# Performance work log

Hardware: AMD Instinct MI355X
Metric: run time of the kernel (lower is better)

Reference implementation:

```python
import jax, jax.numpy as jnp
import numpy as np

DOWNSAMPLE = 4
OUT_RATIO = 8


def _avg_pool(x, k):
    b, c, h, w = x.shape
    return x.reshape(b, c, h // k, k, w // k, k).mean(axis=(3, 5))


def _upsample_axis(x, axis, scale):
    # bilinear, align_corners=True along one axis
    n = x.shape[axis]
    m = n * scale
    coords = jnp.arange(m, dtype=x.dtype) * ((n - 1) / (m - 1))
    i0 = jnp.floor(coords).astype(jnp.int32)
    i1 = jnp.minimum(i0 + 1, n - 1)
    f = coords - i0.astype(x.dtype)
    x0 = jnp.take(x, i0, axis=axis)
    x1 = jnp.take(x, i1, axis=axis)
    shp = [1] * x.ndim
    shp[axis] = m
    f = f.reshape(shp)
    return x0 * (1 - f) + x1 * f


def _upsample_bilinear(x, scale):
    return _upsample_axis(_upsample_axis(x, 2, scale), 3, scale)


def _conv1x1(x, W, b):
    # x: (b,c,h,w), W: (out,in), b: (out,)
    return jnp.einsum('bchw,oc->bohw', x, W) + b[None, :, None, None]


def setup_inputs() -> dict:
    key = jax.random.key(0)
    ks = jax.random.split(key, 8)
    C = 64
    Cq = C // OUT_RATIO
    s = 1.0 / np.sqrt(C)
    x = jax.random.normal(ks[0], (8, C, 256, 256), dtype=jnp.float32)
    Wq = jax.random.uniform(ks[1], (Cq, C), jnp.float32, -s, s)
    bq = jax.random.uniform(ks[2], (Cq,), jnp.float32, -s, s)
    Wk = jax.random.uniform(ks[3], (Cq, C), jnp.float32, -s, s)
    bk = jax.random.uniform(ks[4], (Cq,), jnp.float32, -s, s)
    Wv = jax.random.uniform(ks[5], (C, C), jnp.float32, -s, s)
    bv = jax.random.uniform(ks[6], (C,), jnp.float32, -s, s)
    gamma = jax.random.normal(ks[7], (1,), jnp.float32) * 0.1
    return {"x": x, "Wq": Wq, "bq": bq, "Wk": Wk, "bk": bk, "Wv": Wv, "bv": bv, "gamma": gamma}


def reference(x, Wq, bq, Wk, bk, Wv, bv, gamma):
    b, c, h, w = x.shape
    xd = _avg_pool(x, DOWNSAMPLE)          # (b, c, hd, wd)
    hd, wd = xd.shape[2], xd.shape[3]
    n = hd * wd
    q = _conv1x1(xd, Wq, bq).reshape(b, -1, n)   # (b, cq, n)
    k = _conv1x1(xd, Wk, bk).reshape(b, -1, n)   # (b, cq, n)
    v = _conv1x1(xd, Wv, bv).reshape(b, c, n)    # (b, c, n)
    energy = jnp.einsum('bci,bcj->bij', q, k)    # (b, n, n), no scaling (as in source)
    attn = jax.nn.softmax(energy, axis=-1)
    out = jnp.einsum('bcj,bij->bci', v, attn)    # out[b,c,i] = sum_j v[b,c,j]*attn[b,i,j]
    out = out.reshape(b, c, hd, wd)
    out = _upsample_bilinear(out, DOWNSAMPLE)    # back to (b, c, h, w)
    return gamma[0] * out + x
```

## Files before the change

kernel.cpp:

```cpp
#include <hip/hip_runtime.h>
#include <hip/hip_bf16.h>

#define CCH 64
#define NPIX 4096
#define LOG2E 1.4426950408889634f

typedef __attribute__((ext_vector_type(8))) short short8;
typedef __attribute__((ext_vector_type(16))) float f32x16;

union U4S8 { uint4 u; short8 s; };

__device__ inline uint32_t pk2bf(float lo, float hi) {
    __hip_bfloat162 h = __float22bfloat162_rn(make_float2(lo, hi));
    return *reinterpret_cast<uint32_t*>(&h);
}

__global__ __launch_bounds__(256, 4) void pool_conv_kernel(
    const float* __restrict__ x,
    const float* __restrict__ Wq, const float* __restrict__ bq,
    const float* __restrict__ Wk, const float* __restrict__ bk,
    const float* __restrict__ Wv, const float* __restrict__ bv,
    __hip_bfloat16* __restrict__ Qo, __hip_bfloat16* __restrict__ Ko,
    __hip_bfloat16* __restrict__ VPo)
{
    const int blk  = blockIdx.x;
    const int b    = blk >> 7;
    const int prow = (blk >> 1) & 63;
    const int half = blk & 1;
    const int t    = threadIdx.x;
    const int lane = t & 63;
    const int w    = t >> 6;
    const int l31  = lane & 31;
    const int hi   = lane >> 5;

    __shared__ __align__(16) __hip_bfloat16 xdt[32][72];
    __shared__ __align__(16) __hip_bfloat16 otile[80][36];
    __shared__ float sbias[96];

    if (t < 96) {
        float v = 0.f;
        if (t < 8)       v = bq[t];
        else if (t < 16) v = bk[t-8];
        else if (t < 80) v = bv[t-16];
        sbias[t] = v;
    }

    const float* xbase = x + (((size_t)(b*CCH))*256 + (size_t)(prow*4 + hi))*256
                           + half*128 + l31*4;
    #pragma unroll
    for (int cc = 0; cc < 16; ++cc) {
        const int c = w*16 + cc;
        const float* xp = xbase + (size_t)c*65536;
        float4 a0 = *(const float4*)(xp);
        float4 a1 = *(const float4*)(xp + 512);
        float s = (a0.x+a0.y+a0.z+a0.w) + (a1.x+a1.y+a1.z+a1.w);
        s += __shfl_xor(s, 32);
        if (hi == 0) xdt[l31][c] = __float2bfloat16(s * 0.0625f);
    }

    const int  oct  = w;
    const bool busy = (w < 3);
    short8 wf[4];
    if (busy) {
        const int row = oct*32 + l31;
        const float* wr = nullptr;
        if (row < 8)       wr = Wq + row*CCH;
        else if (row < 16) wr = Wk + (row-8)*CCH;
        else if (row < 80) wr = Wv + (row-16)*CCH;
        #pragma unroll
        for (int kt = 0; kt < 4; ++kt) {
            U4S8 f;
            if (wr) {
                const int c0 = kt*16 + hi*8;
                float4 a = *(const float4*)(wr + c0);
                float4 d = *(const float4*)(wr + c0 + 4);
                f.u.x = pk2bf(a.x, a.y); f.u.y = pk2bf(a.z, a.w);
                f.u.z = pk2bf(d.x, d.y); f.u.w = pk2bf(d.z, d.w);
            } else {
                f.u = make_uint4(0,0,0,0);
            }
            wf[kt] = f.s;
        }
    }

    __syncthreads();

    if (busy) {
        short8 xf[4];
        #pragma unroll
        for (int kt = 0; kt < 4; ++kt)
            xf[kt] = *(const short8*)&xdt[l31][kt*16 + hi*8];

        f32x16 acc;
        #pragma unroll
        for (int r = 0; r < 16; ++r) acc[r] = 0.f;
        #pragma unroll
        for (int kt = 0; kt < 4; ++kt)
            acc = __builtin_amdgcn_mfma_f32_32x32x16_bf16(wf[kt], xf[kt], acc, 0, 0, 0);

        #pragma unroll
        for (int r = 0; r < 16; ++r) {
            const int row = (r&3) + 8*(r>>2) + 4*hi;
            const int oc  = oct*32 + row;
            if (oc < 80) {
                float v = acc[r] + sbias[oc];
                if (oc < 8) v *= LOG2E;
                otile[oc][l31] = __float2bfloat16(v);
            }
        }
    }
    __syncthreads();

    const int i0 = prow*64 + half*32;
    if (t < 64) {
        const int p = t & 31;
        const int oc0 = (t < 32) ? 0 : 8;
        unsigned short v[8];
        #pragma unroll
        for (int j = 0; j < 8; ++j)
            v[j] = *reinterpret_cast<const unsigned short*>(&otile[oc0 + j][p]);
        uint4 q;
        q.x = (uint32_t)v[0] | ((uint32_t)v[1] << 16);
        q.y = (uint32_t)v[2] | ((uint32_t)v[3] << 16);
        q.z = (uint32_t)v[4] | ((uint32_t)v[5] << 16);
        q.w = (uint32_t)v[6] | ((uint32_t)v[7] << 16);
        __hip_bfloat16* dst = (t < 32) ? Qo : Ko;
        *(uint4*)(dst + ((size_t)b*NPIX + i0 + p)*8) = q;
    }
    {
        const int chg = i0 >> 5;
        __hip_bfloat16* vdst = VPo + ((size_t)b*512 + (size_t)chg*4)*512;
        const int f   = t >> 6;
        const int s1  = f >> 1;
        const int ct  = f & 1;
        const int l   = t & 63;
        const int c31 = l & 31;
        const int h2  = l >> 5;
        const int row = 16 + ct*32 + c31;
        const int pt0 = s1*16 + h2*4;
        uint2 a0 = *(const uint2*)&otile[row][pt0];
        uint2 a1 = *(const uint2*)&otile[row][pt0 + 8];
        *(uint4*)(vdst + t*8) = make_uint4(a0.x, a0.y, a1.x, a1.y);
    }
}

__global__ __launch_bounds__(256, 4) void attn_kernel(
    const __hip_bfloat16* __restrict__ Q, const __hip_bfloat16* __restrict__ K,
    const __hip_bfloat16* __restrict__ VP, float* __restrict__ OS)
{
    const int bb   = blockIdx.x;
    const int b    = bb & 7;
    const int qg   = bb >> 3;
    const int i0   = qg * 32;
    const int t    = threadIdx.x;
    const int lane = t & 63;
    const int kvq  = t >> 6;
    const int l31  = lane & 31;
    const int hi   = lane >> 5;

    __shared__ float tiles[4][64][33];
    __shared__ float ml[4][32];
    __shared__ float ils[32];

    U4S8 qf;
    if (hi == 0) qf.u = *(const uint4*)(Q + ((size_t)b*NPIX + i0 + l31)*8);
    else         qf.u = make_uint4(0,0,0,0);

    f32x16 acc0, acc1, zacc;
    #pragma unroll
    for (int r = 0; r < 16; ++r) { acc0[r] = 0.f; acc1[r] = 0.f; zacc[r] = 0.f; }
    float l = 0.f;

    const __hip_bfloat16* Kb  = K  + (size_t)b*NPIX*8;
    const __hip_bfloat16* VPb = VP + (size_t)b*512*512;

    auto ldK = [&](int kv) {
        U4S8 r;
        if (hi == 0) r.u = *(const uint4*)(Kb + (size_t)(kv + l31)*8);
        else         r.u = make_uint4(0,0,0,0);
        return r;
    };
    auto ldVP = [&](int chg, int s1, int ct) {
        U4S8 r;
        r.u = *(const uint4*)(VPb + ((size_t)((chg*2 + s1)*2 + ct))*512 + lane*8);
        return r;
    };

    int kv0 = kvq * 1024;
    U4S8 kf = ldK(kv0);
    U4S8 v00 = ldVP(kv0>>5, 0, 0), v10 = ldVP(kv0>>5, 0, 1);
    U4S8 v01 = ldVP(kv0>>5, 1, 0), v11 = ldVP(kv0>>5, 1, 1);

    #pragma unroll 1
    for (int ch = 0; ch < 32; ++ch) {
        U4S8 ckf = kf, cv00 = v00, cv01 = v01, cv10 = v10, cv11 = v11;
        const int nkv0 = kv0 + 32;
        kf  = ldK(nkv0);
        v00 = ldVP(nkv0>>5, 0, 0); v10 = ldVP(nkv0>>5, 0, 1);
        v01 = ldVP(nkv0>>5, 1, 0); v11 = ldVP(nkv0>>5, 1, 1);

        f32x16 s = __builtin_amdgcn_mfma_f32_32x32x16_bf16(ckf.s, qf.s, zacc, 0, 0, 0);

        float p[16];
        float ssum = 0.f;
        #pragma unroll
        for (int r = 0; r < 16; ++r) { p[r] = __builtin_exp2f(s[r]); ssum += p[r]; }
        l += ssum;

        U4S8 pb0, pb1;
        pb0.u.x = pk2bf(p[0],  p[1]);  pb0.u.y = pk2bf(p[2],  p[3]);
        pb0.u.z = pk2bf(p[4],  p[5]);  pb0.u.w = pk2bf(p[6],  p[7]);
        pb1.u.x = pk2bf(p[8],  p[9]);  pb1.u.y = pk2bf(p[10], p[11]);
        pb1.u.z = pk2bf(p[12], p[13]); pb1.u.w = pk2bf(p[14], p[15]);

        acc0 = __builtin_amdgcn_mfma_f32_32x32x16_bf16(cv00.s, pb0.s, acc0, 0, 0, 0);
        acc1 = __builtin_amdgcn_mfma_f32_32x32x16_bf16(cv10.s, pb0.s, acc1, 0, 0, 0);
        acc0 = __builtin_amdgcn_mfma_f32_32x32x16_bf16(cv01.s, pb1.s, acc0, 0, 0, 0);
        acc1 = __builtin_amdgcn_mfma_f32_32x32x16_bf16(cv11.s, pb1.s, acc1, 0, 0, 0);

        kv0 = nkv0;
    }

    l += __shfl_xor(l, 32);

    #pragma unroll
    for (int r = 0; r < 16; ++r) {
        const int cr = (r&3) + 8*(r>>2) + 4*hi;
        tiles[kvq][cr]     [l31] = acc0[r];
        tiles[kvq][cr + 32][l31] = acc1[r];
    }
    if (hi == 0) ml[kvq][l31] = l;
    __syncthreads();

    if (t < 32) ils[t] = 1.f / (ml[0][t] + ml[1][t] + ml[2][t] + ml[3][t]);
    __syncthreads();

    float* outp = OS + (size_t)b*CCH*NPIX + i0;
    const int c  = t >> 2;
    const int q8 = (t & 3) * 8;
    float o[8];
    #pragma unroll
    for (int j = 0; j < 8; ++j) {
        const int q = q8 + j;
        float v = tiles[0][c][q] + tiles[1][c][q] + tiles[2][c][q] + tiles[3][c][q];
        o[j] = v * ils[q];
    }
    *(float4*)(outp + (size_t)c*NPIX + q8)     = make_float4(o[0], o[1], o[2], o[3]);
    *(float4*)(outp + (size_t)c*NPIX + q8 + 4) = make_float4(o[4], o[5], o[6], o[7]);
}

__global__ __launch_bounds__(256) void upsample_add_kernel(
    const float* __restrict__ OS, const float* __restrict__ x,
    const float* __restrict__ gamma, float* __restrict__ out)
{
    const size_t qidx = (size_t)blockIdx.x * 256 + threadIdx.x;
    const size_t idx  = qidx * 4;
    const float g = gamma[0];
    const int w4 = (int)(idx & 255);
    const int h  = (int)((idx >> 8) & 255);
    const size_t bc = idx >> 16;

    const float scale = 63.0f / 255.0f;
    float fh = h * scale; int h0 = (int)fh; float fy = fh - (float)h0; int h1 = min(h0+1, 63);

    const float* r0 = OS + bc * (size_t)NPIX + h0*64;
    const float* r1 = OS + bc * (size_t)NPIX + h1*64;
    float4 xi = *(const float4*)(x + idx);

    float o[4];
    #pragma unroll
    for (int j = 0; j < 4; ++j) {
        const int w = w4 + j;
        float fw = w * scale; int w0 = (int)fw; float fx = fw - (float)w0; int w1 = min(w0+1, 63);
        float a0 = r0[w0], a1 = r0[w1], b0 = r1[w0], b1 = r1[w1];
        float vt = a0 + (a1 - a0) * fx;
        float vb = b0 + (b1 - b0) * fx;
        o[j] = vt + (vb - vt) * fy;
    }
    float4 ov;
    ov.x = g*o[0] + xi.x; ov.y = g*o[1] + xi.y;
    ov.z = g*o[2] + xi.z; ov.w = g*o[3] + xi.w;
    *(float4*)(out + idx) = ov;
}

extern "C" void kernel_launch(void* const* d_in, const int* in_sizes, int n_in,
                              void* d_out, int out_size, void* d_ws, size_t ws_size,
                              hipStream_t stream) {
    const float* x     = (const float*)d_in[0];
    const float* Wq    = (const float*)d_in[1];
    const float* bq    = (const float*)d_in[2];
    const float* Wk    = (const float*)d_in[3];
    const float* bk    = (const float*)d_in[4];
    const float* Wv    = (const float*)d_in[5];
    const float* bv    = (const float*)d_in[6];
    const float* gamma = (const float*)d_in[7];
    float* out = (float*)d_out;

    char* ws = (char*)d_ws;
    __hip_bfloat16* Qb = (__hip_bfloat16*)(ws);
    __hip_bfloat16* Kb = (__hip_bfloat16*)(ws + (size_t)( 512<<10));
    __hip_bfloat16* VP = (__hip_bfloat16*)(ws + (size_t)(1024<<10));
    float*          OS = (float*)         (ws + (size_t)(5120<<10));

    pool_conv_kernel<<<1024, 256, 0, stream>>>(x, Wq, bq, Wk, bk, Wv, bv, Qb, Kb, VP);
    attn_kernel<<<1024, 256, 0, stream>>>(Qb, Kb, VP, OS);
    const size_t total4 = (size_t)8 * 64 * 256 * 256 / 4;
    upsample_add_kernel<<<(int)(total4 / 256), 256, 0, stream>>>(OS, x, gamma, out);
}
```

Before: 120.4 us.

## Process two query tiles per attention block to reuse K/V loads

Each attention block now handles 64 queries as two 32-query sub-tiles that share the same K and V fragments loaded per chunk, halving the grid to 512 blocks. This is meant to halve global K/V traffic per query and give more independent MFMA/exp work to hide latency. In exchange it doubles the accumulator registers, lowers the occupancy hint to 2 blocks per CU, and leaves half as many blocks to fill the GPU.

```diff
diff --git a/kernel.cpp b/kernel.cpp
--- a/kernel.cpp
+++ b/kernel.cpp
@@ -144,14 +144,14 @@
     }
 }
 
-__global__ __launch_bounds__(256, 4) void attn_kernel(
+__global__ __launch_bounds__(256, 2) void attn_kernel(
     const __hip_bfloat16* __restrict__ Q, const __hip_bfloat16* __restrict__ K,
     const __hip_bfloat16* __restrict__ VP, float* __restrict__ OS)
 {
     const int bb   = blockIdx.x;
     const int b    = bb & 7;
-    const int qg   = bb >> 3;
-    const int i0   = qg * 32;
+    const int qt   = bb >> 3;
+    const int i0   = qt * 64;
     const int t    = threadIdx.x;
     const int lane = t & 63;
     const int kvq  = t >> 6;
@@ -162,14 +162,21 @@
     __shared__ float ml[4][32];
     __shared__ float ils[32];
 
-    U4S8 qf;
-    if (hi == 0) qf.u = *(const uint4*)(Q + ((size_t)b*NPIX + i0 + l31)*8);
-    else         qf.u = make_uint4(0,0,0,0);
-
-    f32x16 acc0, acc1, zacc;
+    U4S8 qfA, qfB;
+    if (hi == 0) {
+        qfA.u = *(const uint4*)(Q + ((size_t)b*NPIX + i0      + l31)*8);
+        qfB.u = *(const uint4*)(Q + ((size_t)b*NPIX + i0 + 32 + l31)*8);
+    } else {
+        qfA.u = make_uint4(0,0,0,0);
+        qfB.u = make_uint4(0,0,0,0);
+    }
+
+    f32x16 accA0, accA1, accB0, accB1, zacc;
     #pragma unroll
-    for (int r = 0; r < 16; ++r) { acc0[r] = 0.f; acc1[r] = 0.f; zacc[r] = 0.f; }
-    float l = 0.f;
+    for (int r = 0; r < 16; ++r) {
+        accA0[r] = 0.f; accA1[r] = 0.f; accB0[r] = 0.f; accB1[r] = 0.f; zacc[r] = 0.f;
+    }
+    float lA = 0.f, lB = 0.f;
 
     const __hip_bfloat16* Kb  = K  + (size_t)b*NPIX*8;
     const __hip_bfloat16* VPb = VP + (size_t)b*512*512;
@@ -199,54 +206,79 @@
         v00 = ldVP(nkv0>>5, 0, 0); v10 = ldVP(nkv0>>5, 0, 1);
         v01 = ldVP(nkv0>>5, 1, 0); v11 = ldVP(nkv0>>5, 1, 1);
 
-        f32x16 s = __builtin_amdgcn_mfma_f32_32x32x16_bf16(ckf.s, qf.s, zacc, 0, 0, 0);
-
-        float p[16];
-        float ssum = 0.f;
-        #pragma unroll
-        for (int r = 0; r < 16; ++r) { p[r] = __builtin_exp2f(s[r]); ssum += p[r]; }
-        l += ssum;
-
-        U4S8 pb0, pb1;
-        pb0.u.x = pk2bf(p[0],  p[1]);  pb0.u.y = pk2bf(p[2],  p[3]);
-        pb0.u.z = pk2bf(p[4],  p[5]);  pb0.u.w = pk2bf(p[6],  p[7]);
-        pb1.u.x = pk2bf(p[8],  p[9]);  pb1.u.y = pk2bf(p[10], p[11]);
-        pb1.u.z = pk2bf(p[12], p[13]); pb1.u.w = pk2bf(p[14], p[15]);
-
-        acc0 = __builtin_amdgcn_mfma_f32_32x32x16_bf16(cv00.s, pb0.s, acc0, 0, 0, 0);
-        acc1 = __builtin_amdgcn_mfma_f32_32x32x16_bf16(cv10.s, pb0.s, acc1, 0, 0, 0);
-        acc0 = __builtin_amdgcn_mfma_f32_32x32x16_bf16(cv01.s, pb1.s, acc0, 0, 0, 0);
-        acc1 = __builtin_amdgcn_mfma_f32_32x32x16_bf16(cv11.s, pb1.s, acc1, 0, 0, 0);
+        {
+            f32x16 s = __builtin_amdgcn_mfma_f32_32x32x16_bf16(ckf.s, qfA.s, zacc, 0, 0, 0);
+            float p[16];
+            float ssum = 0.f;
+            #pragma unroll
+            for (int r = 0; r < 16; ++r) { p[r] = __builtin_exp2f(s[r]); ssum += p[r]; }
+            lA += ssum;
+            U4S8 pb0, pb1;
+            pb0.u.x = pk2bf(p[0],  p[1]);  pb0.u.y = pk2bf(p[2],  p[3]);
+            pb0.u.z = pk2bf(p[4],  p[5]);  pb0.u.w = pk2bf(p[6],  p[7]);
+            pb1.u.x = pk2bf(p[8],  p[9]);  pb1.u.y = pk2bf(p[10], p[11]);
+            pb1.u.z = pk2bf(p[12], p[13]); pb1.u.w = pk2bf(p[14], p[15]);
+            accA0 = __builtin_amdgcn_mfma_f32_32x32x16_bf16(cv00.s, pb0.s, accA0, 0, 0, 0);
+            accA1 = __builtin_amdgcn_mfma_f32_32x32x16_bf16(cv10.s, pb0.s, accA1, 0, 0, 0);
+            accA0 = __builtin_amdgcn_mfma_f32_32x32x16_bf16(cv01.s, pb1.s, accA0, 0, 0, 0);
+            accA1 = __builtin_amdgcn_mfma_f32_32x32x16_bf16(cv11.s, pb1.s, accA1, 0, 0, 0);
+        }
+        {
+            f32x16 s = __builtin_amdgcn_mfma_f32_32x32x16_bf16(ckf.s, qfB.s, zacc, 0, 0, 0);
+            float p[16];
+            float ssum = 0.f;
+            #pragma unroll
+            for (int r = 0; r < 16; ++r) { p[r] = __builtin_exp2f(s[r]); ssum += p[r]; }
+            lB += ssum;
+            U4S8 pb0, pb1;
+            pb0.u.x = pk2bf(p[0],  p[1]);  pb0.u.y = pk2bf(p[2],  p[3]);
+            pb0.u.z = pk2bf(p[4],  p[5]);  pb0.u.w = pk2bf(p[6],  p[7]);
+            pb1.u.x = pk2bf(p[8],  p[9]);  pb1.u.y = pk2bf(p[10], p[11]);
+            pb1.u.z = pk2bf(p[12], p[13]); pb1.u.w = pk2bf(p[14], p[15]);
+            accB0 = __builtin_amdgcn_mfma_f32_32x32x16_bf16(cv00.s, pb0.s, accB0, 0, 0, 0);
+            accB1 = __builtin_amdgcn_mfma_f32_32x32x16_bf16(cv10.s, pb0.s, accB1, 0, 0, 0);
+            accB0 = __builtin_amdgcn_mfma_f32_32x32x16_bf16(cv01.s, pb1.s, accB0, 0, 0, 0);
+            accB1 = __builtin_amdgcn_mfma_f32_32x32x16_bf16(cv11.s, pb1.s, accB1, 0, 0, 0);
+        }
 
         kv0 = nkv0;
     }
 
-    l += __shfl_xor(l, 32);
+    lA += __shfl_xor(lA, 32);
+    lB += __shfl_xor(lB, 32);
 
     #pragma unroll
-    for (int r = 0; r < 16; ++r) {
-        const int cr = (r&3) + 8*(r>>2) + 4*hi;
-        tiles[kvq][cr]     [l31] = acc0[r];
-        tiles[kvq][cr + 32][l31] = acc1[r];
-    }
-    if (hi == 0) ml[kvq][l31] = l;
-    __syncthreads();
-
-    if (t < 32) ils[t] = 1.f / (ml[0][t] + ml[1][t] + ml[2][t] + ml[3][t]);
-    __syncthreads();
-
-    float* outp = OS + (size_t)b*CCH*NPIX + i0;
-    const int c  = t >> 2;
-    const int q8 = (t & 3) * 8;
-    float o[8];
-    #pragma unroll
-    for (int j = 0; j < 8; ++j) {
-        const int q = q8 + j;
-        float v = tiles[0][c][q] + tiles[1][c][q] + tiles[2][c][q] + tiles[3][c][q];
-        o[j] = v * ils[q];
-    }
-    *(float4*)(outp + (size_t)c*NPIX + q8)     = make_float4(o[0], o[1], o[2], o[3]);
-    *(float4*)(outp + (size_t)c*NPIX + q8 + 4) = make_float4(o[4], o[5], o[6], o[7]);
+    for (int g = 0; g < 2; ++g) {
+        if (g == 1) __syncthreads();
+        {
+            const f32x16& a0 = g ? accB0 : accA0;
+            const f32x16& a1 = g ? accB1 : accA1;
+            #pragma unroll
+            for (int r = 0; r < 16; ++r) {
+                const int cr = (r&3) + 8*(r>>2) + 4*hi;
+                tiles[kvq][cr]     [l31] = a0[r];
+                tiles[kvq][cr + 32][l31] = a1[r];
+            }
+            if (hi == 0) ml[kvq][l31] = g ? lB : lA;
+        }
+        __syncthreads();
+
+        if (t < 32) ils[t] = 1.f / (ml[0][t] + ml[1][t] + ml[2][t] + ml[3][t]);
+        __syncthreads();
+
+        float* outp = OS + (size_t)b*CCH*NPIX + i0 + g*32;
+        const int c  = t >> 2;
+        const int q8 = (t & 3) * 8;
+        float o[8];
+        #pragma unroll
+        for (int j = 0; j < 8; ++j) {
+            const int q = q8 + j;
+            float v = tiles[0][c][q] + tiles[1][c][q] + tiles[2][c][q] + tiles[3][c][q];
+            o[j] = v * ils[q];
+        }
+        *(float4*)(outp + (size_t)c*NPIX + q8)     = make_float4(o[0], o[1], o[2], o[3]);
+        *(float4*)(outp + (size_t)c*NPIX + q8 + 4) = make_float4(o[4], o[5], o[6], o[7]);
+    }
 }
 
 __global__ __launch_bounds__(256) void upsample_add_kernel(
@@ -303,7 +335,7 @@
     float*          OS = (float*)         (ws + (size_t)(5120<<10));
 
     pool_conv_kernel<<<1024, 256, 0, stream>>>(x, Wq, bq, Wk, bk, Wv, bv, Qb, Kb, VP);
-    attn_kernel<<<1024, 256, 0, stream>>>(Qb, Kb, VP, OS);
+    attn_kernel<<<512, 256, 0, stream>>>(Qb, Kb, VP, OS);
     const size_t total4 = (size_t)8 * 64 * 256 * 256 / 4;
     upsample_add_kernel<<<(int)(total4 / 256), 256, 0, stream>>>(OS, x, gamma, out);
 }
```

Result: no change. 121.8 us (+1.1%).
